# Kernel tuning notes

Hardware: AMD Instinct MI355X
Metric: run time of the kernel (lower is better)

The kernel has to match this reference:

```python
import jax, jax.numpy as jnp
import numpy as np
from jax import lax

# Module constraint: hidden_dim == state_dim == expand_dim (see broadcasting in original).
H = 128  # hidden_dim
N = 128  # state_dim
E = 128  # expand_dim = hidden_dim * expand_factor (expand_factor=1)
B, L = 4, 1024


def setup_inputs() -> dict:
    key = jax.random.key(0)
    ks = jax.random.split(key, 11)
    s = lambda fan: 1.0 / np.sqrt(fan)
    return {
        "u": jax.random.normal(ks[0], (B, L, H), jnp.float32),
        "W_in": jax.random.normal(ks[1], (H, 2 * E), jnp.float32) * s(H),
        "b_in": jax.random.normal(ks[2], (2 * E,), jnp.float32) * 0.01,
        "conv_w": jax.random.normal(ks[3], (E, 1, 3), jnp.float32) * s(3),
        "conv_b": jax.random.normal(ks[4], (E,), jnp.float32) * 0.01,
        "W_x": jax.random.normal(ks[5], (E, N + N + H), jnp.float32) * s(E),
        "b_x": jax.random.normal(ks[6], (N + N + H,), jnp.float32) * 0.01,
        "A_log": jax.random.normal(ks[7], (N,), jnp.float32),
        "D": jnp.ones((H,), jnp.float32),
        "W_out": jax.random.normal(ks[8], (E, H), jnp.float32) * s(E),
        "b_out": jax.random.normal(ks[9], (H,), jnp.float32) * 0.01,
    }


def reference(u, W_in, b_in, conv_w, conv_b, W_x, b_x, A_log, D, W_out, b_out):
    b, l, _ = u.shape
    xz = u @ W_in + b_in                       # [B,L,2E]
    x, z = jnp.split(xz, 2, axis=-1)           # [B,L,E] each
    # depthwise conv1d, kernel 3, padding 1 (groups == channels)
    xc = lax.conv_general_dilated(
        x.transpose(0, 2, 1), conv_w, window_strides=(1,), padding=[(1, 1)],
        feature_group_count=E, dimension_numbers=("NCH", "OIH", "NCH"))
    x = jax.nn.silu(xc.transpose(0, 2, 1) + conv_b)  # [B,L,E]
    ssm = x @ W_x + b_x                        # [B,L,2N+H]
    delta = jax.nn.softplus(ssm[..., :N])      # [B,L,N]
    Bm = ssm[..., N:2 * N]                     # [B,L,N]
    C = ssm[..., 2 * N:]                       # [B,L,H]
    A = -jnp.exp(A_log)                        # [N]

    def step(h, inp):
        d_t, B_t, C_t, x_t, u_t = inp          # [B,N],[B,N],[B,H],[B,E],[B,H]
        # A_discrete[b,t,i,j] = exp(delta[b,t,i] * A[j])  (outer broadcast, as in source)
        A_disc = jnp.exp(d_t[:, :, None] * A[None, None, :])       # [B,N,N]
        h = A_disc * h + (d_t * B_t)[:, :, None] * x_t[:, None, :]  # [B,N,E]
        y = (h * C_t[:, None, :]).sum(axis=1) + D * u_t             # [B,H]
        return h, y

    h0 = jnp.zeros((b, N, H), u.dtype)
    inputs = (delta.transpose(1, 0, 2), Bm.transpose(1, 0, 2),
              C.transpose(1, 0, 2), x.transpose(1, 0, 2), u.transpose(1, 0, 2))
    _, ys = lax.scan(step, h0, inputs)         # ys: [L,B,H]
    y = ys.transpose(1, 0, 2) * jax.nn.silu(z)  # [B,L,H] (E==H)
    return y @ W_out + b_out                   # dropout in eval mode: identity
```

## Files before the change

### kernel.cpp

```cpp
#include <hip/hip_runtime.h>
#include <hip/hip_bf16.h>

using bf16 = __hip_bfloat16;
typedef __attribute__((ext_vector_type(8))) short short8;
typedef __attribute__((ext_vector_type(4))) float f32x4;

#define BVAL 4
#define LVAL 1024
#define LOG2E 1.44269504f

#define PTS 68

#define OFF_BIN    0
#define OFF_CONVW  256
#define OFF_CONVB  640
#define OFF_BX     768
#define OFF_ALOG   1152
#define OFF_D      1280
#define OFF_BOUT   1408
#define CVT_SMALL  1536

#define R_UBF   524288
#define R_WTIN  (R_UBF + 32768)
#define R_WTX   (R_WTIN + 49152)
#define R_WTOUT (R_WTX + 16384)
#define R_TOT   (R_WTOUT + CVT_SMALL)

__device__ __forceinline__ int dtype_flag(const void* D) {
    return ((*(const unsigned int*)D) & 0xFFFFu) != 0u ? 1 : 0;
}
__device__ __forceinline__ float ldin(const void* p, size_t i, int f) {
    return f ? __bfloat162float(((const bf16*)p)[i]) : ((const float*)p)[i];
}
__device__ __forceinline__ short f2bf(float x) {
    union { bf16 h; short s; } u; u.h = __float2bfloat16(x); return u.s;
}

__global__ void k0_cvt(const void* __restrict__ u, const void* __restrict__ W_in,
                       const void* __restrict__ b_in, const void* __restrict__ conv_w,
                       const void* __restrict__ conv_b, const void* __restrict__ W_x,
                       const void* __restrict__ b_x, const void* __restrict__ A_log,
                       const void* __restrict__ D, const void* __restrict__ W_out,
                       const void* __restrict__ b_out,
                       float* __restrict__ cvt, bf16* __restrict__ ubf,
                       bf16* __restrict__ wtin, bf16* __restrict__ wtx,
                       bf16* __restrict__ wtout) {
    int idx = blockIdx.x * 256 + threadIdx.x;
    if (idx >= R_TOT) return;
    int f = dtype_flag(D);
    if (idx < R_UBF) {
        ubf[idx] = __float2bfloat16(ldin(u, idx, f));
    } else if (idx < R_WTIN) {
        int rel = idx - R_UBF; int n = rel >> 7, k = rel & 127;
        wtin[rel] = __float2bfloat16(ldin(W_in, (size_t)k * 256 + n, f));
    } else if (idx < R_WTX) {
        int rel = idx - R_WTIN; int n = rel >> 7, k = rel & 127;
        wtx[rel] = __float2bfloat16(ldin(W_x, (size_t)k * 384 + n, f));
    } else if (idx < R_WTOUT) {
        int rel = idx - R_WTX; int n = rel >> 7, k = rel & 127;
        wtout[rel] = __float2bfloat16(ldin(W_out, (size_t)k * 128 + n, f));
    } else {
        int rel = idx - R_WTOUT; const void* p; int loc;
        if      (rel < 256)  { p = b_in;   loc = rel; }
        else if (rel < 640)  { p = conv_w; loc = rel - 256; }
        else if (rel < 768)  { p = conv_b; loc = rel - 640; }
        else if (rel < 1152) { p = b_x;    loc = rel - 768; }
        else if (rel < 1280) { p = A_log;  loc = rel - 1152; }
        else if (rel < 1408) { p = D;      loc = rel - 1280; }
        else                 { p = b_out;  loc = rel - 1408; }
        cvt[rel] = ldin(p, loc, f);
    }
}

__global__ void k1_mfma(const bf16* __restrict__ ubf, const bf16* __restrict__ wtin,
                        const float* __restrict__ cvt,
                        float* __restrict__ x_pre, float* __restrict__ zs) {
    int blk = blockIdx.x, mb = blk >> 3, cb = blk & 7;
    int tid = threadIdx.x, w = tid >> 6, lane = tid & 63;
    int quad = lane >> 4, sub = lane & 15;
    int m0 = mb * 64 + w * 16, c = cb * 16;
    f32x4 accX = {0.f, 0.f, 0.f, 0.f}, accZ = {0.f, 0.f, 0.f, 0.f};
    #pragma unroll
    for (int ks = 0; ks < 4; ++ks) {
        int k0 = ks * 32 + quad * 8;
        short8 a  = *(const short8*)(ubf + (size_t)(m0 + sub) * 128 + k0);
        short8 bX = *(const short8*)(wtin + (size_t)(c + sub) * 128 + k0);
        short8 bZ = *(const short8*)(wtin + (size_t)(128 + c + sub) * 128 + k0);
        accX = __builtin_amdgcn_mfma_f32_16x16x32_bf16(a, bX, accX, 0, 0, 0);
        accZ = __builtin_amdgcn_mfma_f32_16x16x32_bf16(a, bZ, accZ, 0, 0, 0);
    }
    int o = c + sub;
    float bx_ = cvt[OFF_BIN + o], bz_ = cvt[OFF_BIN + 128 + o];
    #pragma unroll
    for (int r = 0; r < 4; ++r) {
        int m = m0 + quad * 4 + r;
        float x = accX[r] + bx_;
        float z = accZ[r] + bz_;
        x_pre[(size_t)m * 128 + o] = x;
        zs[(size_t)m * 128 + o] = z / (1.0f + __expf(-z));
    }
}

__global__ void k3_mfma(const float* __restrict__ x_pre, const bf16* __restrict__ wtx,
                        const float* __restrict__ cvt, float* __restrict__ xT,
                        float* __restrict__ dT, float* __restrict__ wT,
                        float* __restrict__ CcT) {
    __shared__ float swc[128 * 4];
    int blk = blockIdx.x, mb = blk >> 3, cb = blk & 7;
    int tid = threadIdx.x, w = tid >> 6, lane = tid & 63;
    int quad = lane >> 4, sub = lane & 15;
    if (tid < 128) {
        swc[tid * 4 + 0] = cvt[OFF_CONVW + tid * 3 + 0];
        swc[tid * 4 + 1] = cvt[OFF_CONVW + tid * 3 + 1];
        swc[tid * 4 + 2] = cvt[OFF_CONVW + tid * 3 + 2];
        swc[tid * 4 + 3] = cvt[OFF_CONVB + tid];
    }
    __syncthreads();
    int m0 = mb * 64 + w * 16, c = cb * 16;
    int row = m0 + sub;
    int l = row & (LVAL - 1);
    const float* xr = x_pre + (size_t)row * 128;
    f32x4 accA = {0.f,0.f,0.f,0.f}, accB = {0.f,0.f,0.f,0.f}, accC = {0.f,0.f,0.f,0.f};
    #pragma unroll
    for (int ks = 0; ks < 4; ++ks) {
        int k0 = ks * 32 + quad * 8;
        float ccv[8], mmv[8], ppv[8];
        *(float4*)&ccv[0] = *(const float4*)(xr + k0);
        *(float4*)&ccv[4] = *(const float4*)(xr + k0 + 4);
        if (l > 0) {
            *(float4*)&mmv[0] = *(const float4*)(xr + k0 - 128);
            *(float4*)&mmv[4] = *(const float4*)(xr + k0 - 124);
        } else {
            #pragma unroll
            for (int i = 0; i < 8; ++i) mmv[i] = 0.f;
        }
        if (l < LVAL - 1) {
            *(float4*)&ppv[0] = *(const float4*)(xr + k0 + 128);
            *(float4*)&ppv[4] = *(const float4*)(xr + k0 + 132);
        } else {
            #pragma unroll
            for (int i = 0; i < 8; ++i) ppv[i] = 0.f;
        }
        float o_[8];
        short8 a;
        #pragma unroll
        for (int i = 0; i < 8; ++i) {
            const float* wc = &swc[(k0 + i) * 4];
            float v = fmaf(wc[0], mmv[i], fmaf(wc[1], ccv[i], fmaf(wc[2], ppv[i], wc[3])));
            o_[i] = v / (1.0f + __expf(-v));
            a[i] = f2bf(o_[i]);
        }
        if (cb == 0) {
            #pragma unroll
            for (int i = 0; i < 8; ++i)
                xT[(size_t)(k0 + i) * 4096 + row] = o_[i];
        }
        short8 bA = *(const short8*)(wtx + (size_t)(c + sub) * 128 + k0);
        short8 bB = *(const short8*)(wtx + (size_t)(128 + c + sub) * 128 + k0);
        short8 bC = *(const short8*)(wtx + (size_t)(256 + c + sub) * 128 + k0);
        accA = __builtin_amdgcn_mfma_f32_16x16x32_bf16(a, bA, accA, 0, 0, 0);
        accB = __builtin_amdgcn_mfma_f32_16x16x32_bf16(a, bB, accB, 0, 0, 0);
        accC = __builtin_amdgcn_mfma_f32_16x16x32_bf16(a, bC, accC, 0, 0, 0);
    }
    int o = c + sub;
    float ba = cvt[OFF_BX + o], bb = cvt[OFF_BX + 128 + o], bc = cvt[OFF_BX + 256 + o];
    float4 spv, dbv, ccv4;
    #pragma unroll
    for (int r = 0; r < 4; ++r) {
        float d = accA[r] + ba;
        float sp = (d > 20.0f) ? d : log1pf(__expf(d));
        ((float*)&spv)[r]  = sp;
        ((float*)&dbv)[r]  = sp * (accB[r] + bb);
        ((float*)&ccv4)[r] = accC[r] + bc;
    }
    int m4 = (m0 >> 2) + quad;
    *(float4*)(dT  + (size_t)m4 * 512 + o * 4)            = spv;
    *(float4*)(wT  + (size_t)m4 * 512 + o * 4)            = dbv;
    *(float4*)(CcT + (size_t)o * 4096 + m0 + quad * 4)    = ccv4;
}


__global__ __launch_bounds__(256, 8)
void k5a_scan(const float* __restrict__ cvt, const float* __restrict__ dT,
              const float* __restrict__ wT, const float* __restrict__ xT,
              float* __restrict__ hfin, float* __restrict__ Pfin) {
    int blk = blockIdx.x;
    int seg = blk & 7, half = (blk >> 3) & 1, jq = (blk >> 4) & 31, b = blk >> 9;
    int tid = threadIdx.x, w = tid >> 6, lane = tid & 63;
    int j = jq * 4 + w, ni = half * 64 + lane;
    int t0 = b * 1024 + seg * 128;
    float a2 = -__expf(cvt[OFF_ALOG + j]) * LOG2E;
    const float4* gd4 = (const float4*)dT + (size_t)(t0 >> 2) * 128 + ni;
    const float4* gw4 = (const float4*)wT + (size_t)(t0 >> 2) * 128 + ni;
    const float4* gx4 = (const float4*)(xT + (size_t)j * 4096 + t0);
    float h = 0.f, sd = 0.f;
#define P1S(dv, wv, xv) { h = fmaf(exp2f((dv) * a2), h, (wv) * (xv)); sd += (dv); }
    for (int c = 0; c < 16; ++c) {
        float4 d0 = gd4[(c * 2 + 0) * 128], d1 = gd4[(c * 2 + 1) * 128];
        float4 w0 = gw4[(c * 2 + 0) * 128], w1 = gw4[(c * 2 + 1) * 128];
        float4 x0 = gx4[c * 2 + 0],         x1 = gx4[c * 2 + 1];
        P1S(d0.x, w0.x, x0.x) P1S(d0.y, w0.y, x0.y)
        P1S(d0.z, w0.z, x0.z) P1S(d0.w, w0.w, x0.w)
        P1S(d1.x, w1.x, x1.x) P1S(d1.y, w1.y, x1.y)
        P1S(d1.z, w1.z, x1.z) P1S(d1.w, w1.w, x1.w)
    }
#undef P1S
    size_t fi = ((size_t)(seg * 4 + b) * 128 + j) * 128 + ni;
    hfin[fi] = h;
    Pfin[fi] = exp2f(sd * a2);
}

__global__ void k5b_comb(const float* __restrict__ hfin, const float* __restrict__ Pfin,
                         float* __restrict__ seeds) {
    int q = blockIdx.x * 256 + threadIdx.x;
    int n = q & 127, j = (q >> 7) & 127, b = q >> 14;
    float s = 0.f;
    #pragma unroll
    for (int seg = 0; seg < 8; ++seg) {
        size_t idx = ((size_t)(seg * 4 + b) * 128 + j) * 128 + n;
        seeds[idx] = s;
        s = fmaf(Pfin[idx], s, hfin[idx]);
    }
}

__global__ __launch_bounds__(256, 8)
void k5c_scan(const float* __restrict__ cvt, const float* __restrict__ dT,
              const float* __restrict__ wT, const float* __restrict__ xT,
              const float* __restrict__ CcT, const float* __restrict__ seeds,
              float* __restrict__ pP0) {
    __shared__ float pt[4][8][PTS];
    const size_t NEc = (size_t)BVAL * LVAL * 128;
    int blk = blockIdx.x;
    int seg = blk & 7, half = (blk >> 3) & 1, jq = (blk >> 4) & 31, b = blk >> 9;
    int tid = threadIdx.x, w = tid >> 6, lane = tid & 63;
    int j = jq * 4 + w, ni = half * 64 + lane;
    int t0 = b * 1024 + seg * 128;
    size_t base = (size_t)b * LVAL * 128;
    float* __restrict__ pP = pP0 + (size_t)half * NEc;
    float a2 = -__expf(cvt[OFF_ALOG + j]) * LOG2E;
    const float4* gd4 = (const float4*)dT + (size_t)(t0 >> 2) * 128 + ni;
    const float4* gw4 = (const float4*)wT + (size_t)(t0 >> 2) * 128 + ni;
    const float4* gx4 = (const float4*)(xT + (size_t)j * 4096 + t0);
    const float*  gcp = CcT + (size_t)j * 4096 + t0;
    float (*ptw)[PTS] = pt[w];
    int rr = lane >> 3, rq = lane & 7;
    float h = seeds[((size_t)(seg * 4 + b) * 128 + j) * 128 + ni];
#define P2S(dv, wv, xv, row) { h = fmaf(exp2f((dv) * a2), h, (wv) * (xv)); \
                               ptw[row][lane] = h; }
    for (int c = 0; c < 16; ++c) {
        float4 d0 = gd4[(c * 2 + 0) * 128], d1 = gd4[(c * 2 + 1) * 128];
        float4 w0 = gw4[(c * 2 + 0) * 128], w1 = gw4[(c * 2 + 1) * 128];
        float4 x0 = gx4[c * 2 + 0],         x1 = gx4[c * 2 + 1];
        float cv = gcp[c * 8 + rr];
        P2S(d0.x, w0.x, x0.x, 0) P2S(d0.y, w0.y, x0.y, 1)
        P2S(d0.z, w0.z, x0.z, 2) P2S(d0.w, w0.w, x0.w, 3)
        P2S(d1.x, w1.x, x1.x, 4) P2S(d1.y, w1.y, x1.y, 5)
        P2S(d1.z, w1.z, x1.z, 6) P2S(d1.w, w1.w, x1.w, 7)
        const float4* pr = (const float4*)&ptw[rr][rq * 8];
        float4 v0 = pr[0], v1 = pr[1];
        float s = ((v0.x + v0.y) + (v0.z + v0.w)) + ((v1.x + v1.y) + (v1.z + v1.w));
        s += __shfl_xor(s, 1, 64);
        s += __shfl_xor(s, 2, 64);
        s += __shfl_xor(s, 4, 64);
        if (rq == 0) {
            int tl = seg * 128 + c * 8 + rr;
            pP[base + (size_t)tl * 128 + j] = cv * s;
        }
    }
#undef P2S
}

__global__ void k6_mfma(const float* __restrict__ pA, const float* __restrict__ pB,
                        const float* __restrict__ zs, const void* __restrict__ uin,
                        const bf16* __restrict__ wtout, const float* __restrict__ cvt,
                        const void* __restrict__ Din, void* __restrict__ out) {
    int blk = blockIdx.x, mb = blk >> 2, nb = blk & 3;
    int tid = threadIdx.x, w = tid >> 6, lane = tid & 63;
    int quad = lane >> 4, sub = lane & 15;
    int m0 = mb * 64 + w * 16, n0 = nb * 32;
    int f = dtype_flag(Din);
    int row = m0 + sub;
    f32x4 acc0 = {0.f,0.f,0.f,0.f}, acc1 = {0.f,0.f,0.f,0.f};
    #pragma unroll
    for (int ks = 0; ks < 4; ++ks) {
        int k0 = ks * 32 + quad * 8;
        size_t ri = (size_t)row * 128 + k0;
        float av[8], bv[8], zv[8], dv[8];
        *(float4*)&av[0] = *(const float4*)(pA + ri);
        *(float4*)&av[4] = *(const float4*)(pA + ri + 4);
        *(float4*)&bv[0] = *(const float4*)(pB + ri);
        *(float4*)&bv[4] = *(const float4*)(pB + ri + 4);
        *(float4*)&zv[0] = *(const float4*)(zs + ri);
        *(float4*)&zv[4] = *(const float4*)(zs + ri + 4);
        *(float4*)&dv[0] = *(const float4*)(cvt + OFF_D + k0);
        *(float4*)&dv[4] = *(const float4*)(cvt + OFF_D + k0 + 4);
        short8 a;
        #pragma unroll
        for (int i = 0; i < 8; ++i) {
            float uu = ldin(uin, ri + i, f);
            float v = (av[i] + bv[i] + dv[i] * uu) * zv[i];
            a[i] = f2bf(v);
        }
        short8 b0 = *(const short8*)(wtout + (size_t)(n0 + sub) * 128 + k0);
        short8 b1 = *(const short8*)(wtout + (size_t)(n0 + 16 + sub) * 128 + k0);
        acc0 = __builtin_amdgcn_mfma_f32_16x16x32_bf16(a, b0, acc0, 0, 0, 0);
        acc1 = __builtin_amdgcn_mfma_f32_16x16x32_bf16(a, b1, acc1, 0, 0, 0);
    }
    float bo0 = cvt[OFF_BOUT + n0 + sub], bo1 = cvt[OFF_BOUT + n0 + 16 + sub];
    #pragma unroll
    for (int r = 0; r < 4; ++r) {
        int m = m0 + quad * 4 + r;
        float v0 = acc0[r] + bo0, v1 = acc1[r] + bo1;
        if (f) {
            ((bf16*)out)[(size_t)m * 128 + n0 + sub] = __float2bfloat16(v0);
            ((bf16*)out)[(size_t)m * 128 + n0 + 16 + sub] = __float2bfloat16(v1);
        } else {
            ((float*)out)[(size_t)m * 128 + n0 + sub] = v0;
            ((float*)out)[(size_t)m * 128 + n0 + 16 + sub] = v1;
        }
    }
}

extern "C" void kernel_launch(void* const* d_in, const int* in_sizes, int n_in,
                              void* d_out, int out_size, void* d_ws, size_t ws_size,
                              hipStream_t stream) {
    const size_t NE = (size_t)BVAL * LVAL * 128;

    float* cvt   = (float*)d_ws;
    float* bufs  = cvt + 2048;
    float* x_pre = bufs + 0 * NE;
    float* zs    = bufs + 1 * NE;
    float* xT    = bufs + 2 * NE;
    float* dT    = bufs + 3 * NE;
    float* wT    = bufs + 4 * NE;
    float* CcT   = bufs + 5 * NE;
    float* pA    = bufs + 6 * NE;
    float* hfin  = bufs + 8 * NE;
    float* Pfin  = bufs + 9 * NE;
    float* seeds = bufs + 10 * NE;
    bf16* ubf    = (bf16*)(bufs + 11 * NE);
    bf16* wtin   = ubf + NE;
    bf16* wtx    = wtin + 32768;
    bf16* wtout  = wtx + 49152;

    k0_cvt<<<(R_TOT + 255) / 256, 256, 0, stream>>>(
        d_in[0], d_in[1], d_in[2], d_in[3], d_in[4], d_in[5],
        d_in[6], d_in[7], d_in[8], d_in[9], d_in[10],
        cvt, ubf, wtin, wtx, wtout);
    k1_mfma<<<512, 256, 0, stream>>>(ubf, wtin, cvt, x_pre, zs);
    k3_mfma<<<512, 256, 0, stream>>>(x_pre, wtx, cvt, xT, dT, wT, CcT);
    k5a_scan<<<2048, 256, 0, stream>>>(cvt, dT, wT, xT, hfin, Pfin);
    k5b_comb<<<256, 256, 0, stream>>>(hfin, Pfin, seeds);
    k5c_scan<<<2048, 256, 0, stream>>>(cvt, dT, wT, xT, CcT, seeds, pA);
    k6_mfma<<<256, 256, 0, stream>>>(pA, pA + NE, zs, d_in[0], wtout, cvt,
                                     d_in[8], d_out);
}
```

Before: 162.2 us.

## Share delta/weight tiles across 8 waves via double-buffered LDS in scan kernels

Both scan kernels now run 512-thread blocks covering 8 j-columns instead of 4. The delta and dB·x weight rows are cooperatively loaded once per block into double-buffered shared memory and read by all 8 waves, instead of each wave loading them from global memory. The next 16-step chunk is prefetched while the current one is processed. This halves redundant global/L2 traffic for dT and wT, at the cost of a block-wide barrier per 16 steps and more LDS per block, which may reduce occupancy.

Result: faster. 156.0 us (-3.8%).

```diff
diff --git a/kernel.cpp b/kernel.cpp
--- a/kernel.cpp
+++ b/kernel.cpp
@@ -180,31 +180,49 @@
 }
 
 
-__global__ __launch_bounds__(256, 8)
+__global__ __launch_bounds__(512, 8)
 void k5a_scan(const float* __restrict__ cvt, const float* __restrict__ dT,
               const float* __restrict__ wT, const float* __restrict__ xT,
               float* __restrict__ hfin, float* __restrict__ Pfin) {
+    __shared__ float sdl[2][16][64], swl[2][16][64];
     int blk = blockIdx.x;
-    int seg = blk & 7, half = (blk >> 3) & 1, jq = (blk >> 4) & 31, b = blk >> 9;
-    int tid = threadIdx.x, w = tid >> 6, lane = tid & 63;
-    int j = jq * 4 + w, ni = half * 64 + lane;
+    int seg = blk & 7, half = (blk >> 3) & 1, jg = (blk >> 4) & 15, b = blk >> 8;
+    int tid = threadIdx.x, w = tid >> 6, lane = tid & 63;
+    int j = jg * 8 + w, ni = half * 64 + lane;
     int t0 = b * 1024 + seg * 128;
     float a2 = -__expf(cvt[OFF_ALOG + j]) * LOG2E;
-    const float4* gd4 = (const float4*)dT + (size_t)(t0 >> 2) * 128 + ni;
-    const float4* gw4 = (const float4*)wT + (size_t)(t0 >> 2) * 128 + ni;
+    int arr = tid >> 8, sq = tid & 255;
+    int sm4 = sq >> 6, sn = sq & 63;
+    const float4* gsrc = (const float4*)(arr ? wT : dT)
+                       + (size_t)(t0 >> 2) * 128 + half * 64 + sn;
     const float4* gx4 = (const float4*)(xT + (size_t)j * 4096 + t0);
     float h = 0.f, sd = 0.f;
-#define P1S(dv, wv, xv) { h = fmaf(exp2f((dv) * a2), h, (wv) * (xv)); sd += (dv); }
-    for (int c = 0; c < 16; ++c) {
-        float4 d0 = gd4[(c * 2 + 0) * 128], d1 = gd4[(c * 2 + 1) * 128];
-        float4 w0 = gw4[(c * 2 + 0) * 128], w1 = gw4[(c * 2 + 1) * 128];
-        float4 x0 = gx4[c * 2 + 0],         x1 = gx4[c * 2 + 1];
-        P1S(d0.x, w0.x, x0.x) P1S(d0.y, w0.y, x0.y)
-        P1S(d0.z, w0.z, x0.z) P1S(d0.w, w0.w, x0.w)
-        P1S(d1.x, w1.x, x1.x) P1S(d1.y, w1.y, x1.y)
-        P1S(d1.z, w1.z, x1.z) P1S(d1.w, w1.w, x1.w)
-    }
-#undef P1S
+    {
+        float4 v = gsrc[sm4 * 128];
+        float* dst = arr ? &swl[0][sm4 * 4][sn] : &sdl[0][sm4 * 4][sn];
+        dst[0] = v.x; dst[64] = v.y; dst[128] = v.z; dst[192] = v.w;
+    }
+    __syncthreads();
+#define A_ST(k, xv) { float dd = sdl[cur][k][lane]; float ww = swl[cur][k][lane]; \
+    h = fmaf(exp2f(dd * a2), h, ww * (xv)); sd += dd; }
+    for (int c = 0; c < 8; ++c) {
+        int cur = c & 1;
+        float4 pf;
+        bool more = (c < 7);
+        if (more) pf = gsrc[((c + 1) * 4 + sm4) * 128];
+        float4 x0 = gx4[c * 4], x1 = gx4[c * 4 + 1];
+        A_ST(0, x0.x) A_ST(1, x0.y) A_ST(2, x0.z) A_ST(3, x0.w)
+        A_ST(4, x1.x) A_ST(5, x1.y) A_ST(6, x1.z) A_ST(7, x1.w)
+        float4 x2 = gx4[c * 4 + 2], x3 = gx4[c * 4 + 3];
+        A_ST(8,  x2.x) A_ST(9,  x2.y) A_ST(10, x2.z) A_ST(11, x2.w)
+        A_ST(12, x3.x) A_ST(13, x3.y) A_ST(14, x3.z) A_ST(15, x3.w)
+        if (more) {
+            float* dst = arr ? &swl[cur ^ 1][sm4 * 4][sn] : &sdl[cur ^ 1][sm4 * 4][sn];
+            dst[0] = pf.x; dst[64] = pf.y; dst[128] = pf.z; dst[192] = pf.w;
+        }
+        __syncthreads();
+    }
+#undef A_ST
     size_t fi = ((size_t)(seg * 4 + b) * 128 + j) * 128 + ni;
     hfin[fi] = h;
     Pfin[fi] = exp2f(sd * a2);
@@ -223,51 +241,70 @@
     }
 }
 
-__global__ __launch_bounds__(256, 8)
+__global__ __launch_bounds__(512, 8)
 void k5c_scan(const float* __restrict__ cvt, const float* __restrict__ dT,
               const float* __restrict__ wT, const float* __restrict__ xT,
               const float* __restrict__ CcT, const float* __restrict__ seeds,
               float* __restrict__ pP0) {
-    __shared__ float pt[4][8][PTS];
+    __shared__ float sdl[2][16][64], swl[2][16][64];
+    __shared__ float pt[8][8][PTS];
     const size_t NEc = (size_t)BVAL * LVAL * 128;
     int blk = blockIdx.x;
-    int seg = blk & 7, half = (blk >> 3) & 1, jq = (blk >> 4) & 31, b = blk >> 9;
-    int tid = threadIdx.x, w = tid >> 6, lane = tid & 63;
-    int j = jq * 4 + w, ni = half * 64 + lane;
+    int seg = blk & 7, half = (blk >> 3) & 1, jg = (blk >> 4) & 15, b = blk >> 8;
+    int tid = threadIdx.x, w = tid >> 6, lane = tid & 63;
+    int j = jg * 8 + w, ni = half * 64 + lane;
     int t0 = b * 1024 + seg * 128;
     size_t base = (size_t)b * LVAL * 128;
     float* __restrict__ pP = pP0 + (size_t)half * NEc;
     float a2 = -__expf(cvt[OFF_ALOG + j]) * LOG2E;
-    const float4* gd4 = (const float4*)dT + (size_t)(t0 >> 2) * 128 + ni;
-    const float4* gw4 = (const float4*)wT + (size_t)(t0 >> 2) * 128 + ni;
+    int arr = tid >> 8, sq = tid & 255;
+    int sm4 = sq >> 6, sn = sq & 63;
+    const float4* gsrc = (const float4*)(arr ? wT : dT)
+                       + (size_t)(t0 >> 2) * 128 + half * 64 + sn;
     const float4* gx4 = (const float4*)(xT + (size_t)j * 4096 + t0);
     const float*  gcp = CcT + (size_t)j * 4096 + t0;
     float (*ptw)[PTS] = pt[w];
     int rr = lane >> 3, rq = lane & 7;
     float h = seeds[((size_t)(seg * 4 + b) * 128 + j) * 128 + ni];
-#define P2S(dv, wv, xv, row) { h = fmaf(exp2f((dv) * a2), h, (wv) * (xv)); \
-                               ptw[row][lane] = h; }
-    for (int c = 0; c < 16; ++c) {
-        float4 d0 = gd4[(c * 2 + 0) * 128], d1 = gd4[(c * 2 + 1) * 128];
-        float4 w0 = gw4[(c * 2 + 0) * 128], w1 = gw4[(c * 2 + 1) * 128];
-        float4 x0 = gx4[c * 2 + 0],         x1 = gx4[c * 2 + 1];
-        float cv = gcp[c * 8 + rr];
-        P2S(d0.x, w0.x, x0.x, 0) P2S(d0.y, w0.y, x0.y, 1)
-        P2S(d0.z, w0.z, x0.z, 2) P2S(d0.w, w0.w, x0.w, 3)
-        P2S(d1.x, w1.x, x1.x, 4) P2S(d1.y, w1.y, x1.y, 5)
-        P2S(d1.z, w1.z, x1.z, 6) P2S(d1.w, w1.w, x1.w, 7)
-        const float4* pr = (const float4*)&ptw[rr][rq * 8];
-        float4 v0 = pr[0], v1 = pr[1];
-        float s = ((v0.x + v0.y) + (v0.z + v0.w)) + ((v1.x + v1.y) + (v1.z + v1.w));
-        s += __shfl_xor(s, 1, 64);
-        s += __shfl_xor(s, 2, 64);
-        s += __shfl_xor(s, 4, 64);
-        if (rq == 0) {
-            int tl = seg * 128 + c * 8 + rr;
-            pP[base + (size_t)tl * 128 + j] = cv * s;
-        }
-    }
-#undef P2S
+    {
+        float4 v = gsrc[sm4 * 128];
+        float* dst = arr ? &swl[0][sm4 * 4][sn] : &sdl[0][sm4 * 4][sn];
+        dst[0] = v.x; dst[64] = v.y; dst[128] = v.z; dst[192] = v.w;
+    }
+    __syncthreads();
+#define C_ST(k, xv) { float dd = sdl[cur][k][lane]; float ww = swl[cur][k][lane]; \
+    h = fmaf(exp2f(dd * a2), h, ww * (xv)); ptw[(k) & 7][lane] = h; }
+#define C_RED(cv, tb) { \
+    const float4* pr_ = (const float4*)&ptw[rr][rq * 8]; \
+    float4 v0_ = pr_[0], v1_ = pr_[1]; \
+    float s_ = ((v0_.x + v0_.y) + (v0_.z + v0_.w)) + ((v1_.x + v1_.y) + (v1_.z + v1_.w)); \
+    s_ += __shfl_xor(s_, 1, 64); \
+    s_ += __shfl_xor(s_, 2, 64); \
+    s_ += __shfl_xor(s_, 4, 64); \
+    if (rq == 0) pP[base + (size_t)((tb) + rr) * 128 + j] = (cv) * s_; }
+    for (int c = 0; c < 8; ++c) {
+        int cur = c & 1;
+        float4 pf;
+        bool more = (c < 7);
+        if (more) pf = gsrc[((c + 1) * 4 + sm4) * 128];
+        float4 x0 = gx4[c * 4], x1 = gx4[c * 4 + 1];
+        float cv0 = gcp[c * 16 + rr];
+        C_ST(0, x0.x) C_ST(1, x0.y) C_ST(2, x0.z) C_ST(3, x0.w)
+        C_ST(4, x1.x) C_ST(5, x1.y) C_ST(6, x1.z) C_ST(7, x1.w)
+        C_RED(cv0, seg * 128 + c * 16)
+        float4 x2 = gx4[c * 4 + 2], x3 = gx4[c * 4 + 3];
+        float cv1 = gcp[c * 16 + 8 + rr];
+        C_ST(8,  x2.x) C_ST(9,  x2.y) C_ST(10, x2.z) C_ST(11, x2.w)
+        C_ST(12, x3.x) C_ST(13, x3.y) C_ST(14, x3.z) C_ST(15, x3.w)
+        C_RED(cv1, seg * 128 + c * 16 + 8)
+        if (more) {
+            float* dst = arr ? &swl[cur ^ 1][sm4 * 4][sn] : &sdl[cur ^ 1][sm4 * 4][sn];
+            dst[0] = pf.x; dst[64] = pf.y; dst[128] = pf.z; dst[192] = pf.w;
+        }
+        __syncthreads();
+    }
+#undef C_ST
+#undef C_RED
 }
 
 __global__ void k6_mfma(const float* __restrict__ pA, const float* __restrict__ pB,
@@ -349,9 +386,9 @@
         cvt, ubf, wtin, wtx, wtout);
     k1_mfma<<<512, 256, 0, stream>>>(ubf, wtin, cvt, x_pre, zs);
     k3_mfma<<<512, 256, 0, stream>>>(x_pre, wtx, cvt, xT, dT, wT, CcT);
-    k5a_scan<<<2048, 256, 0, stream>>>(cvt, dT, wT, xT, hfin, Pfin);
+    k5a_scan<<<1024, 512, 0, stream>>>(cvt, dT, wT, xT, hfin, Pfin);
     k5b_comb<<<256, 256, 0, stream>>>(hfin, Pfin, seeds);
-    k5c_scan<<<2048, 256, 0, stream>>>(cvt, dT, wT, xT, CcT, seeds, pA);
+    k5c_scan<<<1024, 512, 0, stream>>>(cvt, dT, wT, xT, CcT, seeds, pA);
     k6_mfma<<<256, 256, 0, stream>>>(pA, pA + NE, zs, d_in[0], wtout, cvt,
                                      d_in[8], d_out);
 }
```

## Register-block 8 state columns per thread in chunked scan, use 16 segments

Applied to the files above, without the earlier changes.

Each thread in the two scan kernels now carries eight j-columns of state instead of one, so a single load of delta and w is reused eight times. The time axis is split into 16 segments of 64 steps instead of 8 of 128, and the combine kernel and workspace layout are resized to match. The C-weighted reduction in k5c moves to a larger, XOR-swizzled shared-memory tile with a two-lane shuffle. The aim is less redundant global traffic and more independent exp/FMA chains per thread, at the cost of more registers, lower occupancy (launch bounds 8 to 2) and more blocking of the short serial scan.

Measured after the change: 167.0 us. 3.0% more time.

```diff
diff --git a/kernel.cpp b/kernel.cpp
--- a/kernel.cpp
+++ b/kernel.cpp
@@ -8,8 +8,6 @@
 #define BVAL 4
 #define LVAL 1024
 #define LOG2E 1.44269504f
-
-#define PTS 68
 
 #define OFF_BIN    0
 #define OFF_CONVW  256
@@ -180,34 +178,61 @@
 }
 
 
-__global__ __launch_bounds__(256, 8)
+__global__ __launch_bounds__(256, 2)
 void k5a_scan(const float* __restrict__ cvt, const float* __restrict__ dT,
               const float* __restrict__ wT, const float* __restrict__ xT,
               float* __restrict__ hfin, float* __restrict__ Pfin) {
-    int blk = blockIdx.x;
-    int seg = blk & 7, half = (blk >> 3) & 1, jq = (blk >> 4) & 31, b = blk >> 9;
-    int tid = threadIdx.x, w = tid >> 6, lane = tid & 63;
-    int j = jq * 4 + w, ni = half * 64 + lane;
-    int t0 = b * 1024 + seg * 128;
-    float a2 = -__expf(cvt[OFF_ALOG + j]) * LOG2E;
+    int wid = blockIdx.x * 4 + (threadIdx.x >> 6);
+    int lane = threadIdx.x & 63;
+    int jg = wid & 15, half = (wid >> 4) & 1, s = (wid >> 5) & 15, b = wid >> 9;
+    int j0 = jg * 8, ni = half * 64 + lane;
+    int t0 = b * 1024 + s * 64;
+    float a20 = -__expf(cvt[OFF_ALOG + j0 + 0]) * LOG2E;
+    float a21 = -__expf(cvt[OFF_ALOG + j0 + 1]) * LOG2E;
+    float a22 = -__expf(cvt[OFF_ALOG + j0 + 2]) * LOG2E;
+    float a23 = -__expf(cvt[OFF_ALOG + j0 + 3]) * LOG2E;
+    float a24 = -__expf(cvt[OFF_ALOG + j0 + 4]) * LOG2E;
+    float a25 = -__expf(cvt[OFF_ALOG + j0 + 5]) * LOG2E;
+    float a26 = -__expf(cvt[OFF_ALOG + j0 + 6]) * LOG2E;
+    float a27 = -__expf(cvt[OFF_ALOG + j0 + 7]) * LOG2E;
+    float h0=0.f,h1=0.f,h2=0.f,h3=0.f,h4=0.f,h5=0.f,h6=0.f,h7=0.f;
     const float4* gd4 = (const float4*)dT + (size_t)(t0 >> 2) * 128 + ni;
     const float4* gw4 = (const float4*)wT + (size_t)(t0 >> 2) * 128 + ni;
-    const float4* gx4 = (const float4*)(xT + (size_t)j * 4096 + t0);
-    float h = 0.f, sd = 0.f;
-#define P1S(dv, wv, xv) { h = fmaf(exp2f((dv) * a2), h, (wv) * (xv)); sd += (dv); }
+    const float* gxb = xT + (size_t)j0 * 4096 + t0;
+    float sd = 0.f;
+#define A_COMP(F) \
+    h0 = fmaf(exp2f(d4.F * a20), h0, w4.F * xv0.F); \
+    h1 = fmaf(exp2f(d4.F * a21), h1, w4.F * xv1.F); \
+    h2 = fmaf(exp2f(d4.F * a22), h2, w4.F * xv2.F); \
+    h3 = fmaf(exp2f(d4.F * a23), h3, w4.F * xv3.F); \
+    h4 = fmaf(exp2f(d4.F * a24), h4, w4.F * xv4.F); \
+    h5 = fmaf(exp2f(d4.F * a25), h5, w4.F * xv5.F); \
+    h6 = fmaf(exp2f(d4.F * a26), h6, w4.F * xv6.F); \
+    h7 = fmaf(exp2f(d4.F * a27), h7, w4.F * xv7.F);
+    #pragma unroll 2
     for (int c = 0; c < 16; ++c) {
-        float4 d0 = gd4[(c * 2 + 0) * 128], d1 = gd4[(c * 2 + 1) * 128];
-        float4 w0 = gw4[(c * 2 + 0) * 128], w1 = gw4[(c * 2 + 1) * 128];
-        float4 x0 = gx4[c * 2 + 0],         x1 = gx4[c * 2 + 1];
-        P1S(d0.x, w0.x, x0.x) P1S(d0.y, w0.y, x0.y)
-        P1S(d0.z, w0.z, x0.z) P1S(d0.w, w0.w, x0.w)
-        P1S(d1.x, w1.x, x1.x) P1S(d1.y, w1.y, x1.y)
-        P1S(d1.z, w1.z, x1.z) P1S(d1.w, w1.w, x1.w)
-    }
-#undef P1S
-    size_t fi = ((size_t)(seg * 4 + b) * 128 + j) * 128 + ni;
-    hfin[fi] = h;
-    Pfin[fi] = exp2f(sd * a2);
+        float4 d4 = gd4[c * 128], w4 = gw4[c * 128];
+        float4 xv0 = *((const float4*)(gxb + 0 * 4096) + c);
+        float4 xv1 = *((const float4*)(gxb + 1 * 4096) + c);
+        float4 xv2 = *((const float4*)(gxb + 2 * 4096) + c);
+        float4 xv3 = *((const float4*)(gxb + 3 * 4096) + c);
+        float4 xv4 = *((const float4*)(gxb + 4 * 4096) + c);
+        float4 xv5 = *((const float4*)(gxb + 5 * 4096) + c);
+        float4 xv6 = *((const float4*)(gxb + 6 * 4096) + c);
+        float4 xv7 = *((const float4*)(gxb + 7 * 4096) + c);
+        A_COMP(x) A_COMP(y) A_COMP(z) A_COMP(w)
+        sd += (d4.x + d4.y) + (d4.z + d4.w);
+    }
+#undef A_COMP
+    size_t fo = ((size_t)(s * 4 + b) * 128 + j0) * 128 + ni;
+    hfin[fo + 0*128] = h0; Pfin[fo + 0*128] = exp2f(sd * a20);
+    hfin[fo + 1*128] = h1; Pfin[fo + 1*128] = exp2f(sd * a21);
+    hfin[fo + 2*128] = h2; Pfin[fo + 2*128] = exp2f(sd * a22);
+    hfin[fo + 3*128] = h3; Pfin[fo + 3*128] = exp2f(sd * a23);
+    hfin[fo + 4*128] = h4; Pfin[fo + 4*128] = exp2f(sd * a24);
+    hfin[fo + 5*128] = h5; Pfin[fo + 5*128] = exp2f(sd * a25);
+    hfin[fo + 6*128] = h6; Pfin[fo + 6*128] = exp2f(sd * a26);
+    hfin[fo + 7*128] = h7; Pfin[fo + 7*128] = exp2f(sd * a27);
 }
 
 __global__ void k5b_comb(const float* __restrict__ hfin, const float* __restrict__ Pfin,
@@ -216,58 +241,91 @@
     int n = q & 127, j = (q >> 7) & 127, b = q >> 14;
     float s = 0.f;
     #pragma unroll
-    for (int seg = 0; seg < 8; ++seg) {
+    for (int seg = 0; seg < 16; ++seg) {
         size_t idx = ((size_t)(seg * 4 + b) * 128 + j) * 128 + n;
         seeds[idx] = s;
         s = fmaf(Pfin[idx], s, hfin[idx]);
     }
 }
 
-__global__ __launch_bounds__(256, 8)
+__global__ __launch_bounds__(256, 2)
 void k5c_scan(const float* __restrict__ cvt, const float* __restrict__ dT,
               const float* __restrict__ wT, const float* __restrict__ xT,
               const float* __restrict__ CcT, const float* __restrict__ seeds,
               float* __restrict__ pP0) {
-    __shared__ float pt[4][8][PTS];
+    __shared__ float pt[4][4][8][68];
     const size_t NEc = (size_t)BVAL * LVAL * 128;
-    int blk = blockIdx.x;
-    int seg = blk & 7, half = (blk >> 3) & 1, jq = (blk >> 4) & 31, b = blk >> 9;
-    int tid = threadIdx.x, w = tid >> 6, lane = tid & 63;
-    int j = jq * 4 + w, ni = half * 64 + lane;
-    int t0 = b * 1024 + seg * 128;
+    int wid = blockIdx.x * 4 + (threadIdx.x >> 6);
+    int w = (threadIdx.x >> 6) & 3;
+    int lane = threadIdx.x & 63;
+    int jg = wid & 15, half = (wid >> 4) & 1, s = (wid >> 5) & 15, b = wid >> 9;
+    int j0 = jg * 8, ni = half * 64 + lane;
+    int t0 = b * 1024 + s * 64;
     size_t base = (size_t)b * LVAL * 128;
     float* __restrict__ pP = pP0 + (size_t)half * NEc;
-    float a2 = -__expf(cvt[OFF_ALOG + j]) * LOG2E;
+    float a20 = -__expf(cvt[OFF_ALOG + j0 + 0]) * LOG2E;
+    float a21 = -__expf(cvt[OFF_ALOG + j0 + 1]) * LOG2E;
+    float a22 = -__expf(cvt[OFF_ALOG + j0 + 2]) * LOG2E;
+    float a23 = -__expf(cvt[OFF_ALOG + j0 + 3]) * LOG2E;
+    float a24 = -__expf(cvt[OFF_ALOG + j0 + 4]) * LOG2E;
+    float a25 = -__expf(cvt[OFF_ALOG + j0 + 5]) * LOG2E;
+    float a26 = -__expf(cvt[OFF_ALOG + j0 + 6]) * LOG2E;
+    float a27 = -__expf(cvt[OFF_ALOG + j0 + 7]) * LOG2E;
+    size_t fo = ((size_t)(s * 4 + b) * 128 + j0) * 128 + ni;
+    float h0 = seeds[fo + 0*128], h1 = seeds[fo + 1*128];
+    float h2 = seeds[fo + 2*128], h3 = seeds[fo + 3*128];
+    float h4 = seeds[fo + 4*128], h5 = seeds[fo + 5*128];
+    float h6 = seeds[fo + 6*128], h7 = seeds[fo + 7*128];
     const float4* gd4 = (const float4*)dT + (size_t)(t0 >> 2) * 128 + ni;
     const float4* gw4 = (const float4*)wT + (size_t)(t0 >> 2) * 128 + ni;
-    const float4* gx4 = (const float4*)(xT + (size_t)j * 4096 + t0);
-    const float*  gcp = CcT + (size_t)j * 4096 + t0;
-    float (*ptw)[PTS] = pt[w];
-    int rr = lane >> 3, rq = lane & 7;
-    float h = seeds[((size_t)(seg * 4 + b) * 128 + j) * 128 + ni];
-#define P2S(dv, wv, xv, row) { h = fmaf(exp2f((dv) * a2), h, (wv) * (xv)); \
-                               ptw[row][lane] = h; }
+    const float* gxb = xT + (size_t)j0 * 4096 + t0;
+    float (*ptw)[8][68] = pt[w];
+    int p = lane >> 1, hb = lane & 1;
+    int k2 = p >> 3, q2 = p & 7;
+    int sw = (q2 << 2) ^ (k2 << 3);
+    const float* crow = CcT + (size_t)(j0 + q2) * 4096 + t0 + k2;
+#define C_COMP(F, kk) \
+    h0 = fmaf(exp2f(d4.F * a20), h0, w4.F * xv0.F); ptw[kk][0][lane ^ 0  ^ (kk<<3)] = h0; \
+    h1 = fmaf(exp2f(d4.F * a21), h1, w4.F * xv1.F); ptw[kk][1][lane ^ 4  ^ (kk<<3)] = h1; \
+    h2 = fmaf(exp2f(d4.F * a22), h2, w4.F * xv2.F); ptw[kk][2][lane ^ 8  ^ (kk<<3)] = h2; \
+    h3 = fmaf(exp2f(d4.F * a23), h3, w4.F * xv3.F); ptw[kk][3][lane ^ 12 ^ (kk<<3)] = h3; \
+    h4 = fmaf(exp2f(d4.F * a24), h4, w4.F * xv4.F); ptw[kk][4][lane ^ 16 ^ (kk<<3)] = h4; \
+    h5 = fmaf(exp2f(d4.F * a25), h5, w4.F * xv5.F); ptw[kk][5][lane ^ 20 ^ (kk<<3)] = h5; \
+    h6 = fmaf(exp2f(d4.F * a26), h6, w4.F * xv6.F); ptw[kk][6][lane ^ 24 ^ (kk<<3)] = h6; \
+    h7 = fmaf(exp2f(d4.F * a27), h7, w4.F * xv7.F); ptw[kk][7][lane ^ 28 ^ (kk<<3)] = h7;
     for (int c = 0; c < 16; ++c) {
-        float4 d0 = gd4[(c * 2 + 0) * 128], d1 = gd4[(c * 2 + 1) * 128];
-        float4 w0 = gw4[(c * 2 + 0) * 128], w1 = gw4[(c * 2 + 1) * 128];
-        float4 x0 = gx4[c * 2 + 0],         x1 = gx4[c * 2 + 1];
-        float cv = gcp[c * 8 + rr];
-        P2S(d0.x, w0.x, x0.x, 0) P2S(d0.y, w0.y, x0.y, 1)
-        P2S(d0.z, w0.z, x0.z, 2) P2S(d0.w, w0.w, x0.w, 3)
-        P2S(d1.x, w1.x, x1.x, 4) P2S(d1.y, w1.y, x1.y, 5)
-        P2S(d1.z, w1.z, x1.z, 6) P2S(d1.w, w1.w, x1.w, 7)
-        const float4* pr = (const float4*)&ptw[rr][rq * 8];
-        float4 v0 = pr[0], v1 = pr[1];
-        float s = ((v0.x + v0.y) + (v0.z + v0.w)) + ((v1.x + v1.y) + (v1.z + v1.w));
-        s += __shfl_xor(s, 1, 64);
-        s += __shfl_xor(s, 2, 64);
-        s += __shfl_xor(s, 4, 64);
-        if (rq == 0) {
-            int tl = seg * 128 + c * 8 + rr;
-            pP[base + (size_t)tl * 128 + j] = cv * s;
-        }
-    }
-#undef P2S
+        float4 d4 = gd4[c * 128], w4 = gw4[c * 128];
+        float4 xv0 = *((const float4*)(gxb + 0 * 4096) + c);
+        float4 xv1 = *((const float4*)(gxb + 1 * 4096) + c);
+        float4 xv2 = *((const float4*)(gxb + 2 * 4096) + c);
+        float4 xv3 = *((const float4*)(gxb + 3 * 4096) + c);
+        float4 xv4 = *((const float4*)(gxb + 4 * 4096) + c);
+        float4 xv5 = *((const float4*)(gxb + 5 * 4096) + c);
+        float4 xv6 = *((const float4*)(gxb + 6 * 4096) + c);
+        float4 xv7 = *((const float4*)(gxb + 7 * 4096) + c);
+        float cv = crow[c * 4];
+        C_COMP(x, 0) C_COMP(y, 1) C_COMP(z, 2) C_COMP(w, 3)
+        const float* prow = &ptw[k2][q2][0];
+        int cb = hb * 32;
+        float4 v0 = *(const float4*)(prow + (cb + ( 0 ^ sw)));
+        float4 v1 = *(const float4*)(prow + (cb + ( 4 ^ sw)));
+        float4 v2 = *(const float4*)(prow + (cb + ( 8 ^ sw)));
+        float4 v3 = *(const float4*)(prow + (cb + (12 ^ sw)));
+        float4 v4 = *(const float4*)(prow + (cb + (16 ^ sw)));
+        float4 v5 = *(const float4*)(prow + (cb + (20 ^ sw)));
+        float4 v6 = *(const float4*)(prow + (cb + (24 ^ sw)));
+        float4 v7 = *(const float4*)(prow + (cb + (28 ^ sw)));
+        float s_ = (((v0.x+v0.y)+(v0.z+v0.w)) + ((v1.x+v1.y)+(v1.z+v1.w)))
+                 + (((v2.x+v2.y)+(v2.z+v2.w)) + ((v3.x+v3.y)+(v3.z+v3.w)))
+                 + (((v4.x+v4.y)+(v4.z+v4.w)) + ((v5.x+v5.y)+(v5.z+v5.w)))
+                 + (((v6.x+v6.y)+(v6.z+v6.w)) + ((v7.x+v7.y)+(v7.z+v7.w)));
+        s_ += __shfl_xor(s_, 1, 64);
+        if (hb == 0) {
+            int tg = s * 64 + c * 4 + k2;
+            pP[base + (size_t)tg * 128 + j0 + q2] = cv * s_;
+        }
+    }
+#undef C_COMP
 }
 
 __global__ void k6_mfma(const float* __restrict__ pA, const float* __restrict__ pB,
@@ -336,9 +394,9 @@
     float* CcT   = bufs + 5 * NE;
     float* pA    = bufs + 6 * NE;
     float* hfin  = bufs + 8 * NE;
-    float* Pfin  = bufs + 9 * NE;
-    float* seeds = bufs + 10 * NE;
-    bf16* ubf    = (bf16*)(bufs + 11 * NE);
+    float* Pfin  = bufs + 10 * NE;
+    float* seeds = bufs + 12 * NE;
+    bf16* ubf    = (bf16*)(bufs + 14 * NE);
     bf16* wtin   = ubf + NE;
     bf16* wtx    = wtin + 32768;
     bf16* wtout  = wtx + 49152;
@@ -349,9 +407,9 @@
         cvt, ubf, wtin, wtx, wtout);
     k1_mfma<<<512, 256, 0, stream>>>(ubf, wtin, cvt, x_pre, zs);
     k3_mfma<<<512, 256, 0, stream>>>(x_pre, wtx, cvt, xT, dT, wT, CcT);
-    k5a_scan<<<2048, 256, 0, stream>>>(cvt, dT, wT, xT, hfin, Pfin);
+    k5a_scan<<<512, 256, 0, stream>>>(cvt, dT, wT, xT, hfin, Pfin);
     k5b_comb<<<256, 256, 0, stream>>>(hfin, Pfin, seeds);
-    k5c_scan<<<2048, 256, 0, stream>>>(cvt, dT, wT, xT, CcT, seeds, pA);
+    k5c_scan<<<512, 256, 0, stream>>>(cvt, dT, wT, xT, CcT, seeds, pA);
     k6_mfma<<<256, 256, 0, stream>>>(pA, pA + NE, zs, d_in[0], wtout, cvt,
                                      d_in[8], d_out);
 }
```

## Rebalance chunked scan: 4 states per wave, 32 shorter segments, packed carries

Applied to the files above, without the earlier changes.

The chunked scan now gives each wave four j-states and cuts time into 32 segments of 32 steps instead of 8 segments of 128. This shortens the serial dependency chain per thread and reuses each dT/wT load across four states. The segment carries (h, P) are packed into a float2 buffer, and the combine pass walks 32 segments instead of 8. In the second pass the C-weighted reduction uses a new XOR-swizzled shared-memory layout to avoid bank conflicts, in exchange for a longer combine chain and larger seed/carry buffers.

New measurement: 218.4 us. 34.7% more time.

```diff
diff --git a/kernel.cpp b/kernel.cpp
--- a/kernel.cpp
+++ b/kernel.cpp
@@ -8,8 +8,6 @@
 #define BVAL 4
 #define LVAL 1024
 #define LOG2E 1.44269504f
-
-#define PTS 68
 
 #define OFF_BIN    0
 #define OFF_CONVW  256
@@ -183,43 +181,54 @@
 __global__ __launch_bounds__(256, 8)
 void k5a_scan(const float* __restrict__ cvt, const float* __restrict__ dT,
               const float* __restrict__ wT, const float* __restrict__ xT,
-              float* __restrict__ hfin, float* __restrict__ Pfin) {
-    int blk = blockIdx.x;
-    int seg = blk & 7, half = (blk >> 3) & 1, jq = (blk >> 4) & 31, b = blk >> 9;
-    int tid = threadIdx.x, w = tid >> 6, lane = tid & 63;
-    int j = jq * 4 + w, ni = half * 64 + lane;
-    int t0 = b * 1024 + seg * 128;
-    float a2 = -__expf(cvt[OFF_ALOG + j]) * LOG2E;
+              float2* __restrict__ hP) {
+    int wid = blockIdx.x * 4 + (threadIdx.x >> 6);
+    int lane = threadIdx.x & 63;
+    int jg = wid & 31, half = (wid >> 5) & 1, s = (wid >> 6) & 31, b = wid >> 11;
+    int j0 = jg * 4, ni = half * 64 + lane;
+    int t0 = b * 1024 + s * 32;
+    float a20 = -__expf(cvt[OFF_ALOG + j0 + 0]) * LOG2E;
+    float a21 = -__expf(cvt[OFF_ALOG + j0 + 1]) * LOG2E;
+    float a22 = -__expf(cvt[OFF_ALOG + j0 + 2]) * LOG2E;
+    float a23 = -__expf(cvt[OFF_ALOG + j0 + 3]) * LOG2E;
+    float h0 = 0.f, h1 = 0.f, h2 = 0.f, h3 = 0.f, sd = 0.f;
     const float4* gd4 = (const float4*)dT + (size_t)(t0 >> 2) * 128 + ni;
     const float4* gw4 = (const float4*)wT + (size_t)(t0 >> 2) * 128 + ni;
-    const float4* gx4 = (const float4*)(xT + (size_t)j * 4096 + t0);
-    float h = 0.f, sd = 0.f;
-#define P1S(dv, wv, xv) { h = fmaf(exp2f((dv) * a2), h, (wv) * (xv)); sd += (dv); }
-    for (int c = 0; c < 16; ++c) {
-        float4 d0 = gd4[(c * 2 + 0) * 128], d1 = gd4[(c * 2 + 1) * 128];
-        float4 w0 = gw4[(c * 2 + 0) * 128], w1 = gw4[(c * 2 + 1) * 128];
-        float4 x0 = gx4[c * 2 + 0],         x1 = gx4[c * 2 + 1];
-        P1S(d0.x, w0.x, x0.x) P1S(d0.y, w0.y, x0.y)
-        P1S(d0.z, w0.z, x0.z) P1S(d0.w, w0.w, x0.w)
-        P1S(d1.x, w1.x, x1.x) P1S(d1.y, w1.y, x1.y)
-        P1S(d1.z, w1.z, x1.z) P1S(d1.w, w1.w, x1.w)
-    }
-#undef P1S
-    size_t fi = ((size_t)(seg * 4 + b) * 128 + j) * 128 + ni;
-    hfin[fi] = h;
-    Pfin[fi] = exp2f(sd * a2);
-}
-
-__global__ void k5b_comb(const float* __restrict__ hfin, const float* __restrict__ Pfin,
-                         float* __restrict__ seeds) {
+    const float4* gx0 = (const float4*)(xT + (size_t)(j0 + 0) * 4096 + t0);
+    const float4* gx1 = (const float4*)(xT + (size_t)(j0 + 1) * 4096 + t0);
+    const float4* gx2 = (const float4*)(xT + (size_t)(j0 + 2) * 4096 + t0);
+    const float4* gx3 = (const float4*)(xT + (size_t)(j0 + 3) * 4096 + t0);
+#define A_COMP(F) \
+    h0 = fmaf(exp2f(d4.F * a20), h0, w4.F * xv0.F); \
+    h1 = fmaf(exp2f(d4.F * a21), h1, w4.F * xv1.F); \
+    h2 = fmaf(exp2f(d4.F * a22), h2, w4.F * xv2.F); \
+    h3 = fmaf(exp2f(d4.F * a23), h3, w4.F * xv3.F);
+    #pragma unroll
+    for (int c = 0; c < 8; ++c) {
+        float4 d4 = gd4[c * 128], w4 = gw4[c * 128];
+        float4 xv0 = gx0[c], xv1 = gx1[c], xv2 = gx2[c], xv3 = gx3[c];
+        A_COMP(x) A_COMP(y) A_COMP(z) A_COMP(w)
+        sd += (d4.x + d4.y) + (d4.z + d4.w);
+    }
+#undef A_COMP
+    size_t fo = (size_t)(s * 4 + b) * 16384 + (size_t)j0 * 128 + ni;
+    hP[fo + 0 * 128] = make_float2(h0, exp2f(sd * a20));
+    hP[fo + 1 * 128] = make_float2(h1, exp2f(sd * a21));
+    hP[fo + 2 * 128] = make_float2(h2, exp2f(sd * a22));
+    hP[fo + 3 * 128] = make_float2(h3, exp2f(sd * a23));
+}
+
+__global__ __launch_bounds__(256, 4)
+void k5b_comb(const float2* __restrict__ hP, float* __restrict__ seeds) {
     int q = blockIdx.x * 256 + threadIdx.x;
     int n = q & 127, j = (q >> 7) & 127, b = q >> 14;
     float s = 0.f;
     #pragma unroll
-    for (int seg = 0; seg < 8; ++seg) {
-        size_t idx = ((size_t)(seg * 4 + b) * 128 + j) * 128 + n;
+    for (int seg = 0; seg < 32; ++seg) {
+        size_t idx = (size_t)(seg * 4 + b) * 16384 + (size_t)j * 128 + n;
         seeds[idx] = s;
-        s = fmaf(Pfin[idx], s, hfin[idx]);
+        float2 hp = hP[idx];
+        s = fmaf(hp.y, s, hp.x);
     }
 }
 
@@ -228,46 +237,60 @@
               const float* __restrict__ wT, const float* __restrict__ xT,
               const float* __restrict__ CcT, const float* __restrict__ seeds,
               float* __restrict__ pP0) {
-    __shared__ float pt[4][8][PTS];
+    __shared__ float pt[4][4][4][68];
     const size_t NEc = (size_t)BVAL * LVAL * 128;
-    int blk = blockIdx.x;
-    int seg = blk & 7, half = (blk >> 3) & 1, jq = (blk >> 4) & 31, b = blk >> 9;
-    int tid = threadIdx.x, w = tid >> 6, lane = tid & 63;
-    int j = jq * 4 + w, ni = half * 64 + lane;
-    int t0 = b * 1024 + seg * 128;
+    int w = (threadIdx.x >> 6) & 3;
+    int wid = blockIdx.x * 4 + (threadIdx.x >> 6);
+    int lane = threadIdx.x & 63;
+    int jg = wid & 31, half = (wid >> 5) & 1, s = (wid >> 6) & 31, b = wid >> 11;
+    int j0 = jg * 4, ni = half * 64 + lane;
+    int t0 = b * 1024 + s * 32;
     size_t base = (size_t)b * LVAL * 128;
     float* __restrict__ pP = pP0 + (size_t)half * NEc;
-    float a2 = -__expf(cvt[OFF_ALOG + j]) * LOG2E;
+    float a20 = -__expf(cvt[OFF_ALOG + j0 + 0]) * LOG2E;
+    float a21 = -__expf(cvt[OFF_ALOG + j0 + 1]) * LOG2E;
+    float a22 = -__expf(cvt[OFF_ALOG + j0 + 2]) * LOG2E;
+    float a23 = -__expf(cvt[OFF_ALOG + j0 + 3]) * LOG2E;
+    size_t fo = (size_t)(s * 4 + b) * 16384 + (size_t)j0 * 128 + ni;
+    float h0 = seeds[fo + 0 * 128], h1 = seeds[fo + 1 * 128];
+    float h2 = seeds[fo + 2 * 128], h3 = seeds[fo + 3 * 128];
     const float4* gd4 = (const float4*)dT + (size_t)(t0 >> 2) * 128 + ni;
     const float4* gw4 = (const float4*)wT + (size_t)(t0 >> 2) * 128 + ni;
-    const float4* gx4 = (const float4*)(xT + (size_t)j * 4096 + t0);
-    const float*  gcp = CcT + (size_t)j * 4096 + t0;
-    float (*ptw)[PTS] = pt[w];
-    int rr = lane >> 3, rq = lane & 7;
-    float h = seeds[((size_t)(seg * 4 + b) * 128 + j) * 128 + ni];
-#define P2S(dv, wv, xv, row) { h = fmaf(exp2f((dv) * a2), h, (wv) * (xv)); \
-                               ptw[row][lane] = h; }
-    for (int c = 0; c < 16; ++c) {
-        float4 d0 = gd4[(c * 2 + 0) * 128], d1 = gd4[(c * 2 + 1) * 128];
-        float4 w0 = gw4[(c * 2 + 0) * 128], w1 = gw4[(c * 2 + 1) * 128];
-        float4 x0 = gx4[c * 2 + 0],         x1 = gx4[c * 2 + 1];
-        float cv = gcp[c * 8 + rr];
-        P2S(d0.x, w0.x, x0.x, 0) P2S(d0.y, w0.y, x0.y, 1)
-        P2S(d0.z, w0.z, x0.z, 2) P2S(d0.w, w0.w, x0.w, 3)
-        P2S(d1.x, w1.x, x1.x, 4) P2S(d1.y, w1.y, x1.y, 5)
-        P2S(d1.z, w1.z, x1.z, 6) P2S(d1.w, w1.w, x1.w, 7)
-        const float4* pr = (const float4*)&ptw[rr][rq * 8];
-        float4 v0 = pr[0], v1 = pr[1];
-        float s = ((v0.x + v0.y) + (v0.z + v0.w)) + ((v1.x + v1.y) + (v1.z + v1.w));
-        s += __shfl_xor(s, 1, 64);
-        s += __shfl_xor(s, 2, 64);
-        s += __shfl_xor(s, 4, 64);
-        if (rq == 0) {
-            int tl = seg * 128 + c * 8 + rr;
-            pP[base + (size_t)tl * 128 + j] = cv * s;
-        }
-    }
-#undef P2S
+    const float4* gx0 = (const float4*)(xT + (size_t)(j0 + 0) * 4096 + t0);
+    const float4* gx1 = (const float4*)(xT + (size_t)(j0 + 1) * 4096 + t0);
+    const float4* gx2 = (const float4*)(xT + (size_t)(j0 + 2) * 4096 + t0);
+    const float4* gx3 = (const float4*)(xT + (size_t)(j0 + 3) * 4096 + t0);
+    float (*ptw)[4][68] = pt[w];
+    int hb = lane & 3, p = lane >> 2;
+    int k2 = p >> 2, q2 = p & 3;
+    int sw = (q2 << 2) ^ (k2 << 4);
+    const float* crow = CcT + (size_t)(j0 + q2) * 4096 + t0 + k2;
+#define C_COMP(F, kk) \
+    h0 = fmaf(exp2f(d4.F * a20), h0, w4.F * xv0.F); ptw[kk][0][lane ^ 0  ^ ((kk) << 4)] = h0; \
+    h1 = fmaf(exp2f(d4.F * a21), h1, w4.F * xv1.F); ptw[kk][1][lane ^ 4  ^ ((kk) << 4)] = h1; \
+    h2 = fmaf(exp2f(d4.F * a22), h2, w4.F * xv2.F); ptw[kk][2][lane ^ 8  ^ ((kk) << 4)] = h2; \
+    h3 = fmaf(exp2f(d4.F * a23), h3, w4.F * xv3.F); ptw[kk][3][lane ^ 12 ^ ((kk) << 4)] = h3;
+    #pragma unroll
+    for (int g = 0; g < 8; ++g) {
+        float4 d4 = gd4[g * 128], w4 = gw4[g * 128];
+        float4 xv0 = gx0[g], xv1 = gx1[g], xv2 = gx2[g], xv3 = gx3[g];
+        float cv = crow[g * 4];
+        C_COMP(x, 0) C_COMP(y, 1) C_COMP(z, 2) C_COMP(w, 3)
+        const float* prow = &ptw[k2][q2][0];
+        float4 v0 = *(const float4*)(prow + ((hb * 16 + 0)  ^ sw));
+        float4 v1 = *(const float4*)(prow + ((hb * 16 + 4)  ^ sw));
+        float4 v2 = *(const float4*)(prow + ((hb * 16 + 8)  ^ sw));
+        float4 v3 = *(const float4*)(prow + ((hb * 16 + 12) ^ sw));
+        float s_ = (((v0.x + v0.y) + (v0.z + v0.w)) + ((v1.x + v1.y) + (v1.z + v1.w)))
+                 + (((v2.x + v2.y) + (v2.z + v2.w)) + ((v3.x + v3.y) + (v3.z + v3.w)));
+        s_ += __shfl_xor(s_, 1, 64);
+        s_ += __shfl_xor(s_, 2, 64);
+        if (hb == 0) {
+            int tl = s * 32 + g * 4 + k2;
+            pP[base + (size_t)tl * 128 + j0 + q2] = cv * s_;
+        }
+    }
+#undef C_COMP
 }
 
 __global__ void k6_mfma(const float* __restrict__ pA, const float* __restrict__ pB,
@@ -335,10 +358,9 @@
     float* wT    = bufs + 4 * NE;
     float* CcT   = bufs + 5 * NE;
     float* pA    = bufs + 6 * NE;
-    float* hfin  = bufs + 8 * NE;
-    float* Pfin  = bufs + 9 * NE;
-    float* seeds = bufs + 10 * NE;
-    bf16* ubf    = (bf16*)(bufs + 11 * NE);
+    float2* hP   = (float2*)(bufs + 8 * NE);
+    float* seeds = bufs + 16 * NE;
+    bf16* ubf    = (bf16*)(bufs + 20 * NE);
     bf16* wtin   = ubf + NE;
     bf16* wtx    = wtin + 32768;
     bf16* wtout  = wtx + 49152;
@@ -349,8 +371,8 @@
         cvt, ubf, wtin, wtx, wtout);
     k1_mfma<<<512, 256, 0, stream>>>(ubf, wtin, cvt, x_pre, zs);
     k3_mfma<<<512, 256, 0, stream>>>(x_pre, wtx, cvt, xT, dT, wT, CcT);
-    k5a_scan<<<2048, 256, 0, stream>>>(cvt, dT, wT, xT, hfin, Pfin);
-    k5b_comb<<<256, 256, 0, stream>>>(hfin, Pfin, seeds);
+    k5a_scan<<<2048, 256, 0, stream>>>(cvt, dT, wT, xT, hP);
+    k5b_comb<<<256, 256, 0, stream>>>(hP, seeds);
     k5c_scan<<<2048, 256, 0, stream>>>(cvt, dT, wT, xT, CcT, seeds, pA);
     k6_mfma<<<256, 256, 0, stream>>>(pA, pA + NE, zs, d_in[0], wtout, cvt,
                                      d_in[8], d_out);
```
